# Performance work log

Measured on AMD Instinct MI355X. Metric: run time of the kernel, lower is better.

The kernel has to match this reference:

```python
import jax, jax.numpy as jnp
import numpy as np

N = 8192
D_IN = 32
HIDDEN = [32, 32, 32]   # -> 2 GraphConvolution layers
FC = [32, 1]            # hfc = [32, 32, 1] -> 2 Linear layers


def _uniform(key, shape, stdv):
    return jax.random.uniform(key, shape, jnp.float32, -stdv, stdv)


def setup_inputs() -> dict:
    key = jax.random.key(0)
    ks = jax.random.split(key, 32)
    inp = {}
    inp["V"] = jax.random.normal(ks[0], (N, D_IN), jnp.float32)
    inp["adj"] = jax.random.randint(ks[1], (N, N), 0, 4, jnp.int32)
    # GCN layer params: w1, w2, w3 [in, out], bias [out]; init U(-stdv, stdv), stdv = 1/sqrt(out)
    ki = 2
    for li in range(len(HIDDEN) - 1):
        a, b = HIDDEN[li], HIDDEN[li + 1]
        stdv = 1.0 / np.sqrt(b)
        for wname in ("w1", "w2", "w3"):
            inp[f"{wname}_{li}"] = _uniform(ks[ki], (a, b), stdv); ki += 1
        inp[f"gb_{li}"] = _uniform(ks[ki], (b,), stdv); ki += 1
    # FC params (torch Linear default init: U(-1/sqrt(in), 1/sqrt(in)))
    hfc = [HIDDEN[-1]] + FC
    for li in range(len(hfc) - 1):
        a, b = hfc[li], hfc[li + 1]
        stdv = 1.0 / np.sqrt(a)
        inp[f"fcW_{li}"] = _uniform(ks[ki], (b, a), stdv); ki += 1  # torch Linear weight is [out, in]
        inp[f"fcb_{li}"] = _uniform(ks[ki], (b,), stdv); ki += 1
    return inp


def _gcn(V, adj, w1, w2, w3, bias):
    # masked-adjacency relational aggregation: sum_k (adj==k) @ (V @ w_k)
    dt = V.dtype
    o = (adj == 1).astype(dt) @ (V @ w1)
    o = o + (adj == 2).astype(dt) @ (V @ w2)
    o = o + (adj == 3).astype(dt) @ (V @ w3)
    return jax.nn.relu(o + bias)


def reference(V, adj, w1_0, w2_0, w3_0, gb_0, w1_1, w2_1, w3_1, gb_1,
              fcW_0, fcb_0, fcW_1, fcb_1):
    Z = _gcn(V, adj, w1_0, w2_0, w3_0, gb_0)          # [N, 32]
    Z = _gcn(Z, adj, w1_1, w2_1, w3_1, gb_1)          # [N, 32]
    Z = jnp.sum(Z, axis=0)                             # [32] sum pooling over nodes
    Z = jax.nn.relu(Z @ fcW_0.T + fcb_0)               # dropout = identity (eval mode)
    Z = Z @ fcW_1.T + fcb_1                            # [1]
    return jax.nn.sigmoid(Z)
```

## Files before the change

### kernel.cpp

```cpp
#include <hip/hip_runtime.h>
#include <cmath>

#define NN 8192

typedef _Float16 half8 __attribute__((ext_vector_type(8)));
typedef float floatx4 __attribute__((ext_vector_type(4)));
typedef unsigned int uint;

template <int L2>
__global__ __launch_bounds__(256) void h_kernel(
    const float* __restrict__ X, const float* __restrict__ w1,
    const float* __restrict__ w2, const float* __restrict__ w3,
    const float* __restrict__ gbias, _Float16* __restrict__ Hfrag) {
  __shared__ float wl[32][32];
  __shared__ float Xs[64][32];
  const int tid = threadIdx.x;
  const int ch = blockIdx.y;
  const float* wsrc = (ch == 0) ? w1 : (ch == 1) ? w2 : w3;
  for (int i = tid; i < 1024; i += 256) ((float*)wl)[i] = wsrc[i];
  const size_t base = (size_t)blockIdx.x * 2048 + tid * 8;
  if (L2 == 0) {
    float4 x0 = ((const float4*)(X + base))[0];
    float4 x1 = ((const float4*)(X + base))[1];
    *((float4*)(&Xs[0][0] + tid * 8)) = x0;
    *((float4*)(&Xs[0][0] + tid * 8 + 4)) = x1;
  } else {
    float4 s0 = {0.f, 0.f, 0.f, 0.f}, s1 = {0.f, 0.f, 0.f, 0.f};
#pragma unroll
    for (int c = 0; c < 8; ++c) {
      const float4* p = (const float4*)(X + (size_t)c * NN * 32 + base);
      float4 a = p[0], b = p[1];
      s0.x += a.x; s0.y += a.y; s0.z += a.z; s0.w += a.w;
      s1.x += b.x; s1.y += b.y; s1.z += b.z; s1.w += b.w;
    }
    const int c0 = (tid * 8) & 31;
    const float4 b0 = *(const float4*)(gbias + c0);
    const float4 b1 = *(const float4*)(gbias + c0 + 4);
    s0.x += b0.x; s0.y += b0.y; s0.z += b0.z; s0.w += b0.w;
    s1.x += b1.x; s1.y += b1.y; s1.z += b1.z; s1.w += b1.w;
    s0.x = s0.x > 0.f ? s0.x : 0.f; s0.y = s0.y > 0.f ? s0.y : 0.f;
    s0.z = s0.z > 0.f ? s0.z : 0.f; s0.w = s0.w > 0.f ? s0.w : 0.f;
    s1.x = s1.x > 0.f ? s1.x : 0.f; s1.y = s1.y > 0.f ? s1.y : 0.f;
    s1.z = s1.z > 0.f ? s1.z : 0.f; s1.w = s1.w > 0.f ? s1.w : 0.f;
    *((float4*)(&Xs[0][0] + tid * 8)) = s0;
    *((float4*)(&Xs[0][0] + tid * 8 + 4)) = s1;
  }
  __syncthreads();
  const int n = tid & 31, jb = tid >> 5;
  const int j0 = blockIdx.x * 64 + jb * 8;
  const int t = j0 >> 5;
  const int lane = (n & 15) | (((j0 & 31) >> 3) << 4);
  const int tile = n >> 4;
  half8 hv;
#pragma unroll
  for (int jj = 0; jj < 8; ++jj) {
    const float4* xr = (const float4*)(&Xs[jb * 8 + jj][0]);
    float acc = 0.f;
#pragma unroll
    for (int d4 = 0; d4 < 8; ++d4) {
      float4 x = xr[d4];
      acc += x.x * wl[d4 * 4 + 0][n];
      acc += x.y * wl[d4 * 4 + 1][n];
      acc += x.z * wl[d4 * 4 + 2][n];
      acc += x.w * wl[d4 * 4 + 3][n];
    }
    hv[jj] = (_Float16)acc;
  }
  size_t idx = ((((size_t)ch * 256 + t) * 2 + tile) * 64 + lane) * 8;
  *(half8*)(Hfrag + idx) = hv;
}

__device__ __forceinline__ void phaseB_core(const uint* mk,
                                            const half8* __restrict__ Hf,
                                            float* red_raw,
                                            float* __restrict__ Zpart, int rg,
                                            int c, int tid) {
  const int w = tid >> 6, lane = tid & 63;
  const int m = lane & 15, q = lane >> 4;
  const half8* hp = Hf + (size_t)(c * 32 + w * 8) * 128 + lane;
  half8 b00 = hp[0],     b01 = hp[64];
  half8 b10 = hp[32768], b11 = hp[32768 + 64];
  half8 b20 = hp[65536], b21 = hp[65536 + 64];
  floatx4 acc00 = {0.f, 0.f, 0.f, 0.f}, acc01 = {0.f, 0.f, 0.f, 0.f};
  floatx4 acc10 = {0.f, 0.f, 0.f, 0.f}, acc11 = {0.f, 0.f, 0.f, 0.f};
#pragma unroll
  for (int tl = 0; tl < 8; ++tl) {
    half8 n00, n01, n10, n11, n20, n21;
    if (tl < 7) {
      const half8* np = hp + (tl + 1) * 128;
      n00 = np[0];     n01 = np[64];
      n10 = np[32768]; n11 = np[32768 + 64];
      n20 = np[65536]; n21 = np[65536 + 64];
    }
    const uint pk = mk[tl];
    half8 a1r0, a2r0, a3r0, a1r1, a2r1, a3r1;
#pragma unroll
    for (int i = 0; i < 8; ++i) {
      const int p0 = (pk >> (2 * i)) & 3;
      const int p1 = (pk >> (16 + 2 * i)) & 3;
      a1r0[i] = (p0 == 1) ? (_Float16)1.f : (_Float16)0.f;
      a2r0[i] = (p0 == 2) ? (_Float16)1.f : (_Float16)0.f;
      a3r0[i] = (p0 == 3) ? (_Float16)1.f : (_Float16)0.f;
      a1r1[i] = (p1 == 1) ? (_Float16)1.f : (_Float16)0.f;
      a2r1[i] = (p1 == 2) ? (_Float16)1.f : (_Float16)0.f;
      a3r1[i] = (p1 == 3) ? (_Float16)1.f : (_Float16)0.f;
    }
    acc00 = __builtin_amdgcn_mfma_f32_16x16x32_f16(a1r0, b00, acc00, 0, 0, 0);
    acc00 = __builtin_amdgcn_mfma_f32_16x16x32_f16(a2r0, b10, acc00, 0, 0, 0);
    acc00 = __builtin_amdgcn_mfma_f32_16x16x32_f16(a3r0, b20, acc00, 0, 0, 0);
    acc01 = __builtin_amdgcn_mfma_f32_16x16x32_f16(a1r0, b01, acc01, 0, 0, 0);
    acc01 = __builtin_amdgcn_mfma_f32_16x16x32_f16(a2r0, b11, acc01, 0, 0, 0);
    acc01 = __builtin_amdgcn_mfma_f32_16x16x32_f16(a3r0, b21, acc01, 0, 0, 0);
    acc10 = __builtin_amdgcn_mfma_f32_16x16x32_f16(a1r1, b00, acc10, 0, 0, 0);
    acc10 = __builtin_amdgcn_mfma_f32_16x16x32_f16(a2r1, b10, acc10, 0, 0, 0);
    acc10 = __builtin_amdgcn_mfma_f32_16x16x32_f16(a3r1, b20, acc10, 0, 0, 0);
    acc11 = __builtin_amdgcn_mfma_f32_16x16x32_f16(a1r1, b01, acc11, 0, 0, 0);
    acc11 = __builtin_amdgcn_mfma_f32_16x16x32_f16(a2r1, b11, acc11, 0, 0, 0);
    acc11 = __builtin_amdgcn_mfma_f32_16x16x32_f16(a3r1, b21, acc11, 0, 0, 0);
    if (tl < 7) {
      b00 = n00; b01 = n01; b10 = n10; b11 = n11; b20 = n20; b21 = n21;
    }
  }
  float (*red)[4][64][4] = (float (*)[4][64][4])red_raw;
#pragma unroll
  for (int r = 0; r < 4; ++r) {
    red[w][0][lane][r] = acc00[r];
    red[w][1][lane][r] = acc01[r];
    red[w][2][lane][r] = acc10[r];
    red[w][3][lane][r] = acc11[r];
  }
  __syncthreads();
  if (w == 0) {
    const int rbase = rg * 32;
#pragma unroll
    for (int r = 0; r < 4; ++r) {
      const float c00 = red[0][0][lane][r] + red[1][0][lane][r] +
                        red[2][0][lane][r] + red[3][0][lane][r];
      const float c01 = red[0][1][lane][r] + red[1][1][lane][r] +
                        red[2][1][lane][r] + red[3][1][lane][r];
      const float c10 = red[0][2][lane][r] + red[1][2][lane][r] +
                        red[2][2][lane][r] + red[3][2][lane][r];
      const float c11 = red[0][3][lane][r] + red[1][3][lane][r] +
                        red[2][3][lane][r] + red[3][3][lane][r];
      const int ro0 = rbase + q * 4 + r;
      float* zp0 = Zpart + ((size_t)c * NN + ro0) * 32;
      zp0[m] = c00;
      zp0[16 + m] = c01;
      float* zp1 = Zpart + ((size_t)c * NN + ro0 + 16) * 32;
      zp1[m] = c10;
      zp1[16 + m] = c11;
    }
  }
}

__global__ __launch_bounds__(256, 4) void agg1_kernel(
    const int* __restrict__ adj, uint* __restrict__ packed_g,
    const half8* __restrict__ Hf, float* __restrict__ Zpart) {
  __shared__ char smraw[16384];
  uint* ptile = (uint*)smraw;
  const int tid = threadIdx.x;
  const int rg = blockIdx.x >> 3, c = blockIdx.x & 7;
  const int tg = tid >> 5;
  const int qt = (tid >> 1) & 3;
  const int t4 = (tid >> 3) & 3;
  const int ih = tid & 1;
  const int byte_base = tg * 1024 + qt * 256 + t4 * 4 + ih;
  unsigned char* pb = (unsigned char*)ptile;
  const size_t gofs = (size_t)rg * 32 * NN + c * 1024 + tid * 4;
#pragma unroll
  for (int r0 = 0; r0 < 32; r0 += 8) {
    int4 a[8];
#pragma unroll
    for (int rr = 0; rr < 8; ++rr)
      a[rr] = *(const int4*)(adj + gofs + (size_t)(r0 + rr) * NN);
#pragma unroll
    for (int rr = 0; rr < 8; ++rr) {
      const int r = r0 + rr;
      const uint b = (uint)(a[rr].x & 3) | ((uint)(a[rr].y & 3) << 2) |
                     ((uint)(a[rr].z & 3) << 4) | ((uint)(a[rr].w & 3) << 6);
      pb[byte_base + (r & 15) * 16 + (r >> 4) * 2] = (unsigned char)b;
    }
  }
  __syncthreads();
  uint* pg = packed_g + (size_t)blockIdx.x * 2048;
  *(uint4*)(pg + tid * 8) = *(const uint4*)(ptile + tid * 8);
  *(uint4*)(pg + tid * 8 + 4) = *(const uint4*)(ptile + tid * 8 + 4);
  const int w = tid >> 6, lane = tid & 63;
  uint mk[8];
  *(uint4*)(mk) = *(const uint4*)(ptile + (w * 2) * 256 + lane * 4);
  *(uint4*)(mk + 4) = *(const uint4*)(ptile + (w * 2 + 1) * 256 + lane * 4);
  __syncthreads();
  phaseB_core(mk, Hf, (float*)smraw, Zpart, rg, c, tid);
}

__global__ __launch_bounds__(256, 4) void agg2_kernel(
    const uint* __restrict__ packed_g, const half8* __restrict__ Hf,
    float* __restrict__ Zpart) {
  __shared__ float red_lds[4][4][64][4];
  const int tid = threadIdx.x;
  const int rg = blockIdx.x >> 3, c = blockIdx.x & 7;
  const int w = tid >> 6, lane = tid & 63;
  const uint* pg =
      packed_g + (size_t)blockIdx.x * 2048 + (w * 2) * 256 + lane * 4;
  uint mk[8];
  *(uint4*)(mk) = *(const uint4*)(pg);
  *(uint4*)(mk + 4) = *(const uint4*)(pg + 256);
  phaseB_core(mk, Hf, (float*)red_lds, Zpart, rg, c, tid);
}

__global__ __launch_bounds__(256) void pool_kernel(
    const float* __restrict__ Zpart, const float* __restrict__ bias,
    float* __restrict__ partials) {
  const int tid = threadIdx.x;
  const int col = tid & 31, ro = tid >> 5;
  const float b = bias[col];
  float s = 0.f;
  for (int rr = 0; rr < 32; ++rr) {
    const size_t r = (size_t)blockIdx.x * 256 + ro * 32 + rr;
    float v = b;
#pragma unroll
    for (int c = 0; c < 8; ++c) v += Zpart[(size_t)c * NN * 32 + r * 32 + col];
    s += v > 0.f ? v : 0.f;
  }
  __shared__ float red[8][32];
  red[ro][col] = s;
  __syncthreads();
  if (tid < 32) {
    float t = 0.f;
#pragma unroll
    for (int i = 0; i < 8; ++i) t += red[i][tid];
    partials[(size_t)blockIdx.x * 32 + tid] = t;
  }
}

__global__ __launch_bounds__(256) void fc_kernel(
    const float* __restrict__ partials, int np, const float* __restrict__ W0,
    const float* __restrict__ b0, const float* __restrict__ W1,
    const float* __restrict__ b1, float* __restrict__ out) {
  __shared__ float acc8[8][32];
  __shared__ float z[32], y[32];
  const int tid = threadIdx.x;
  const int col = tid & 31, ch = tid >> 5;
  float s = 0.f;
  for (int i = ch; i < np; i += 8) s += partials[(size_t)i * 32 + col];
  acc8[ch][col] = s;
  __syncthreads();
  if (tid < 32) {
    float t = 0.f;
#pragma unroll
    for (int i = 0; i < 8; ++i) t += acc8[i][tid];
    z[tid] = t;
  }
  __syncthreads();
  if (tid < 32) {
    float acc = b0[tid];
    for (int n = 0; n < 32; ++n) acc += W0[tid * 32 + n] * z[n];
    y[tid] = acc > 0.f ? acc : 0.f;
  }
  __syncthreads();
  if (tid == 0) {
    float acc = b1[0];
    for (int mm = 0; mm < 32; ++mm) acc += W1[mm] * y[mm];
    out[0] = 1.f / (1.f + expf(-acc));
  }
}

extern "C" void kernel_launch(void* const* d_in, const int* in_sizes, int n_in,
                              void* d_out, int out_size, void* d_ws,
                              size_t ws_size, hipStream_t stream) {
  const float* V   = (const float*)d_in[0];
  const int*   adj = (const int*)d_in[1];
  const float *w10 = (const float*)d_in[2], *w20 = (const float*)d_in[3],
              *w30 = (const float*)d_in[4], *gb0 = (const float*)d_in[5];
  const float *w11 = (const float*)d_in[6], *w21 = (const float*)d_in[7],
              *w31 = (const float*)d_in[8], *gb1 = (const float*)d_in[9];
  const float *fW0 = (const float*)d_in[10], *fb0 = (const float*)d_in[11],
              *fW1 = (const float*)d_in[12], *fb1 = (const float*)d_in[13];
  float* out = (float*)d_out;
  char* ws = (char*)d_ws;

  _Float16* Hfrag    = (_Float16*)ws;
  float*    Zpart    = (float*)(ws + 1572864);
  float*    partials = (float*)(ws + 9961472);
  uint*     packed   = (uint*)(ws + 10223616);

  h_kernel<0><<<dim3(128, 3), 256, 0, stream>>>(V, w10, w20, w30, nullptr,
                                                Hfrag);
  agg1_kernel<<<2048, 256, 0, stream>>>(adj, packed, (const half8*)Hfrag,
                                        Zpart);
  h_kernel<1><<<dim3(128, 3), 256, 0, stream>>>(Zpart, w11, w21, w31, gb0,
                                                Hfrag);
  agg2_kernel<<<2048, 256, 0, stream>>>(packed, (const half8*)Hfrag, Zpart);
  pool_kernel<<<32, 256, 0, stream>>>(Zpart, gb1, partials);
  fc_kernel<<<1, 256, 0, stream>>>(partials, 32, fW0, fb0, fW1, fb1, out);
}
```

Measured before the change: 440.4 us.

## Split adjacency packing from aggregation and process two row groups per block

The adjacency packing, which reads the 256MB int32 adj, moves into its own pack_kernel with higher occupancy, and one shared agg_kernel now serves both layers. Each aggregation block covers 64 rows instead of 32, so every B fragment of H loaded from memory feeds twice as many MFMAs and the grid is halved. The costs are an extra launch, loss of the overlap between adj reading and MFMA work that agg1 had, and more accumulator registers and LDS per block.

```diff
diff --git a/kernel.cpp b/kernel.cpp
--- a/kernel.cpp
+++ b/kernel.cpp
@@ -70,94 +70,9 @@
   *(half8*)(Hfrag + idx) = hv;
 }
 
-__device__ __forceinline__ void phaseB_core(const uint* mk,
-                                            const half8* __restrict__ Hf,
-                                            float* red_raw,
-                                            float* __restrict__ Zpart, int rg,
-                                            int c, int tid) {
-  const int w = tid >> 6, lane = tid & 63;
-  const int m = lane & 15, q = lane >> 4;
-  const half8* hp = Hf + (size_t)(c * 32 + w * 8) * 128 + lane;
-  half8 b00 = hp[0],     b01 = hp[64];
-  half8 b10 = hp[32768], b11 = hp[32768 + 64];
-  half8 b20 = hp[65536], b21 = hp[65536 + 64];
-  floatx4 acc00 = {0.f, 0.f, 0.f, 0.f}, acc01 = {0.f, 0.f, 0.f, 0.f};
-  floatx4 acc10 = {0.f, 0.f, 0.f, 0.f}, acc11 = {0.f, 0.f, 0.f, 0.f};
-#pragma unroll
-  for (int tl = 0; tl < 8; ++tl) {
-    half8 n00, n01, n10, n11, n20, n21;
-    if (tl < 7) {
-      const half8* np = hp + (tl + 1) * 128;
-      n00 = np[0];     n01 = np[64];
-      n10 = np[32768]; n11 = np[32768 + 64];
-      n20 = np[65536]; n21 = np[65536 + 64];
-    }
-    const uint pk = mk[tl];
-    half8 a1r0, a2r0, a3r0, a1r1, a2r1, a3r1;
-#pragma unroll
-    for (int i = 0; i < 8; ++i) {
-      const int p0 = (pk >> (2 * i)) & 3;
-      const int p1 = (pk >> (16 + 2 * i)) & 3;
-      a1r0[i] = (p0 == 1) ? (_Float16)1.f : (_Float16)0.f;
-      a2r0[i] = (p0 == 2) ? (_Float16)1.f : (_Float16)0.f;
-      a3r0[i] = (p0 == 3) ? (_Float16)1.f : (_Float16)0.f;
-      a1r1[i] = (p1 == 1) ? (_Float16)1.f : (_Float16)0.f;
-      a2r1[i] = (p1 == 2) ? (_Float16)1.f : (_Float16)0.f;
-      a3r1[i] = (p1 == 3) ? (_Float16)1.f : (_Float16)0.f;
-    }
-    acc00 = __builtin_amdgcn_mfma_f32_16x16x32_f16(a1r0, b00, acc00, 0, 0, 0);
-    acc00 = __builtin_amdgcn_mfma_f32_16x16x32_f16(a2r0, b10, acc00, 0, 0, 0);
-    acc00 = __builtin_amdgcn_mfma_f32_16x16x32_f16(a3r0, b20, acc00, 0, 0, 0);
-    acc01 = __builtin_amdgcn_mfma_f32_16x16x32_f16(a1r0, b01, acc01, 0, 0, 0);
-    acc01 = __builtin_amdgcn_mfma_f32_16x16x32_f16(a2r0, b11, acc01, 0, 0, 0);
-    acc01 = __builtin_amdgcn_mfma_f32_16x16x32_f16(a3r0, b21, acc01, 0, 0, 0);
-    acc10 = __builtin_amdgcn_mfma_f32_16x16x32_f16(a1r1, b00, acc10, 0, 0, 0);
-    acc10 = __builtin_amdgcn_mfma_f32_16x16x32_f16(a2r1, b10, acc10, 0, 0, 0);
-    acc10 = __builtin_amdgcn_mfma_f32_16x16x32_f16(a3r1, b20, acc10, 0, 0, 0);
-    acc11 = __builtin_amdgcn_mfma_f32_16x16x32_f16(a1r1, b01, acc11, 0, 0, 0);
-    acc11 = __builtin_amdgcn_mfma_f32_16x16x32_f16(a2r1, b11, acc11, 0, 0, 0);
-    acc11 = __builtin_amdgcn_mfma_f32_16x16x32_f16(a3r1, b21, acc11, 0, 0, 0);
-    if (tl < 7) {
-      b00 = n00; b01 = n01; b10 = n10; b11 = n11; b20 = n20; b21 = n21;
-    }
-  }
-  float (*red)[4][64][4] = (float (*)[4][64][4])red_raw;
-#pragma unroll
-  for (int r = 0; r < 4; ++r) {
-    red[w][0][lane][r] = acc00[r];
-    red[w][1][lane][r] = acc01[r];
-    red[w][2][lane][r] = acc10[r];
-    red[w][3][lane][r] = acc11[r];
-  }
-  __syncthreads();
-  if (w == 0) {
-    const int rbase = rg * 32;
-#pragma unroll
-    for (int r = 0; r < 4; ++r) {
-      const float c00 = red[0][0][lane][r] + red[1][0][lane][r] +
-                        red[2][0][lane][r] + red[3][0][lane][r];
-      const float c01 = red[0][1][lane][r] + red[1][1][lane][r] +
-                        red[2][1][lane][r] + red[3][1][lane][r];
-      const float c10 = red[0][2][lane][r] + red[1][2][lane][r] +
-                        red[2][2][lane][r] + red[3][2][lane][r];
-      const float c11 = red[0][3][lane][r] + red[1][3][lane][r] +
-                        red[2][3][lane][r] + red[3][3][lane][r];
-      const int ro0 = rbase + q * 4 + r;
-      float* zp0 = Zpart + ((size_t)c * NN + ro0) * 32;
-      zp0[m] = c00;
-      zp0[16 + m] = c01;
-      float* zp1 = Zpart + ((size_t)c * NN + ro0 + 16) * 32;
-      zp1[m] = c10;
-      zp1[16 + m] = c11;
-    }
-  }
-}
-
-__global__ __launch_bounds__(256, 4) void agg1_kernel(
-    const int* __restrict__ adj, uint* __restrict__ packed_g,
-    const half8* __restrict__ Hf, float* __restrict__ Zpart) {
-  __shared__ char smraw[16384];
-  uint* ptile = (uint*)smraw;
+__global__ __launch_bounds__(256, 8) void pack_kernel(
+    const int* __restrict__ adj, uint* __restrict__ packed_g) {
+  __shared__ uint ptile[2048];
   const int tid = threadIdx.x;
   const int rg = blockIdx.x >> 3, c = blockIdx.x & 7;
   const int tg = tid >> 5;
@@ -185,27 +100,121 @@
   uint* pg = packed_g + (size_t)blockIdx.x * 2048;
   *(uint4*)(pg + tid * 8) = *(const uint4*)(ptile + tid * 8);
   *(uint4*)(pg + tid * 8 + 4) = *(const uint4*)(ptile + tid * 8 + 4);
-  const int w = tid >> 6, lane = tid & 63;
-  uint mk[8];
-  *(uint4*)(mk) = *(const uint4*)(ptile + (w * 2) * 256 + lane * 4);
-  *(uint4*)(mk + 4) = *(const uint4*)(ptile + (w * 2 + 1) * 256 + lane * 4);
-  __syncthreads();
-  phaseB_core(mk, Hf, (float*)smraw, Zpart, rg, c, tid);
-}
-
-__global__ __launch_bounds__(256, 4) void agg2_kernel(
+}
+
+__global__ __launch_bounds__(256, 4) void agg_kernel(
     const uint* __restrict__ packed_g, const half8* __restrict__ Hf,
     float* __restrict__ Zpart) {
-  __shared__ float red_lds[4][4][64][4];
+  __shared__ float red[4][8][64][4];
   const int tid = threadIdx.x;
   const int rg = blockIdx.x >> 3, c = blockIdx.x & 7;
   const int w = tid >> 6, lane = tid & 63;
-  const uint* pg =
-      packed_g + (size_t)blockIdx.x * 2048 + (w * 2) * 256 + lane * 4;
-  uint mk[8];
-  *(uint4*)(mk) = *(const uint4*)(pg);
-  *(uint4*)(mk + 4) = *(const uint4*)(pg + 256);
-  phaseB_core(mk, Hf, (float*)red_lds, Zpart, rg, c, tid);
+  const int m = lane & 15, q = lane >> 4;
+  const uint* pgA =
+      packed_g + ((size_t)(rg * 2) * 8 + c) * 2048 + (w * 2) * 256 + lane * 4;
+  const uint* pgB =
+      packed_g + ((size_t)(rg * 2 + 1) * 8 + c) * 2048 + (w * 2) * 256 + lane * 4;
+  uint mkA[8], mkB[8];
+  *(uint4*)(mkA) = *(const uint4*)(pgA);
+  *(uint4*)(mkA + 4) = *(const uint4*)(pgA + 256);
+  *(uint4*)(mkB) = *(const uint4*)(pgB);
+  *(uint4*)(mkB + 4) = *(const uint4*)(pgB + 256);
+  const half8* hp = Hf + (size_t)(c * 32 + w * 8) * 128 + lane;
+  half8 b00 = hp[0],     b01 = hp[64];
+  half8 b10 = hp[32768], b11 = hp[32768 + 64];
+  half8 b20 = hp[65536], b21 = hp[65536 + 64];
+  floatx4 acc[4][2];
+#pragma unroll
+  for (int g = 0; g < 4; ++g)
+#pragma unroll
+    for (int h = 0; h < 2; ++h) acc[g][h] = (floatx4){0.f, 0.f, 0.f, 0.f};
+#pragma unroll
+  for (int tl = 0; tl < 8; ++tl) {
+    half8 n00, n01, n10, n11, n20, n21;
+    if (tl < 7) {
+      const half8* np = hp + (tl + 1) * 128;
+      n00 = np[0];     n01 = np[64];
+      n10 = np[32768]; n11 = np[32768 + 64];
+      n20 = np[65536]; n21 = np[65536 + 64];
+    }
+    const uint pkA = mkA[tl], pkB = mkB[tl];
+    {
+      half8 a0, a1, a2, a3;
+#pragma unroll
+      for (int i = 0; i < 8; ++i) {
+        a0[i] = (((pkA >> (2 * i)) & 3) == 1) ? (_Float16)1.f : (_Float16)0.f;
+        a1[i] = (((pkA >> (16 + 2 * i)) & 3) == 1) ? (_Float16)1.f : (_Float16)0.f;
+        a2[i] = (((pkB >> (2 * i)) & 3) == 1) ? (_Float16)1.f : (_Float16)0.f;
+        a3[i] = (((pkB >> (16 + 2 * i)) & 3) == 1) ? (_Float16)1.f : (_Float16)0.f;
+      }
+      acc[0][0] = __builtin_amdgcn_mfma_f32_16x16x32_f16(a0, b00, acc[0][0], 0, 0, 0);
+      acc[0][1] = __builtin_amdgcn_mfma_f32_16x16x32_f16(a0, b01, acc[0][1], 0, 0, 0);
+      acc[1][0] = __builtin_amdgcn_mfma_f32_16x16x32_f16(a1, b00, acc[1][0], 0, 0, 0);
+      acc[1][1] = __builtin_amdgcn_mfma_f32_16x16x32_f16(a1, b01, acc[1][1], 0, 0, 0);
+      acc[2][0] = __builtin_amdgcn_mfma_f32_16x16x32_f16(a2, b00, acc[2][0], 0, 0, 0);
+      acc[2][1] = __builtin_amdgcn_mfma_f32_16x16x32_f16(a2, b01, acc[2][1], 0, 0, 0);
+      acc[3][0] = __builtin_amdgcn_mfma_f32_16x16x32_f16(a3, b00, acc[3][0], 0, 0, 0);
+      acc[3][1] = __builtin_amdgcn_mfma_f32_16x16x32_f16(a3, b01, acc[3][1], 0, 0, 0);
+    }
+    {
+      half8 a0, a1, a2, a3;
+#pragma unroll
+      for (int i = 0; i < 8; ++i) {
+        a0[i] = (((pkA >> (2 * i)) & 3) == 2) ? (_Float16)1.f : (_Float16)0.f;
+        a1[i] = (((pkA >> (16 + 2 * i)) & 3) == 2) ? (_Float16)1.f : (_Float16)0.f;
+        a2[i] = (((pkB >> (2 * i)) & 3) == 2) ? (_Float16)1.f : (_Float16)0.f;
+        a3[i] = (((pkB >> (16 + 2 * i)) & 3) == 2) ? (_Float16)1.f : (_Float16)0.f;
+      }
+      acc[0][0] = __builtin_amdgcn_mfma_f32_16x16x32_f16(a0, b10, acc[0][0], 0, 0, 0);
+      acc[0][1] = __builtin_amdgcn_mfma_f32_16x16x32_f16(a0, b11, acc[0][1], 0, 0, 0);
+      acc[1][0] = __builtin_amdgcn_mfma_f32_16x16x32_f16(a1, b10, acc[1][0], 0, 0, 0);
+      acc[1][1] = __builtin_amdgcn_mfma_f32_16x16x32_f16(a1, b11, acc[1][1], 0, 0, 0);
+      acc[2][0] = __builtin_amdgcn_mfma_f32_16x16x32_f16(a2, b10, acc[2][0], 0, 0, 0);
+      acc[2][1] = __builtin_amdgcn_mfma_f32_16x16x32_f16(a2, b11, acc[2][1], 0, 0, 0);
+      acc[3][0] = __builtin_amdgcn_mfma_f32_16x16x32_f16(a3, b10, acc[3][0], 0, 0, 0);
+      acc[3][1] = __builtin_amdgcn_mfma_f32_16x16x32_f16(a3, b11, acc[3][1], 0, 0, 0);
+    }
+    {
+      half8 a0, a1, a2, a3;
+#pragma unroll
+      for (int i = 0; i < 8; ++i) {
+        a0[i] = (((pkA >> (2 * i)) & 3) == 3) ? (_Float16)1.f : (_Float16)0.f;
+        a1[i] = (((pkA >> (16 + 2 * i)) & 3) == 3) ? (_Float16)1.f : (_Float16)0.f;
+        a2[i] = (((pkB >> (2 * i)) & 3) == 3) ? (_Float16)1.f : (_Float16)0.f;
+        a3[i] = (((pkB >> (16 + 2 * i)) & 3) == 3) ? (_Float16)1.f : (_Float16)0.f;
+      }
+      acc[0][0] = __builtin_amdgcn_mfma_f32_16x16x32_f16(a0, b20, acc[0][0], 0, 0, 0);
+      acc[0][1] = __builtin_amdgcn_mfma_f32_16x16x32_f16(a0, b21, acc[0][1], 0, 0, 0);
+      acc[1][0] = __builtin_amdgcn_mfma_f32_16x16x32_f16(a1, b20, acc[1][0], 0, 0, 0);
+      acc[1][1] = __builtin_amdgcn_mfma_f32_16x16x32_f16(a1, b21, acc[1][1], 0, 0, 0);
+      acc[2][0] = __builtin_amdgcn_mfma_f32_16x16x32_f16(a2, b20, acc[2][0], 0, 0, 0);
+      acc[2][1] = __builtin_amdgcn_mfma_f32_16x16x32_f16(a2, b21, acc[2][1], 0, 0, 0);
+      acc[3][0] = __builtin_amdgcn_mfma_f32_16x16x32_f16(a3, b20, acc[3][0], 0, 0, 0);
+      acc[3][1] = __builtin_amdgcn_mfma_f32_16x16x32_f16(a3, b21, acc[3][1], 0, 0, 0);
+    }
+    if (tl < 7) {
+      b00 = n00; b01 = n01; b10 = n10; b11 = n11; b20 = n20; b21 = n21;
+    }
+  }
+#pragma unroll
+  for (int g = 0; g < 4; ++g)
+#pragma unroll
+    for (int h = 0; h < 2; ++h)
+#pragma unroll
+      for (int r = 0; r < 4; ++r) red[w][g * 2 + h][lane][r] = acc[g][h][r];
+  __syncthreads();
+  {
+    const int rbase = rg * 64 + w * 16;
+#pragma unroll
+    for (int h = 0; h < 2; ++h) {
+#pragma unroll
+      for (int r = 0; r < 4; ++r) {
+        const float v = red[0][w * 2 + h][lane][r] + red[1][w * 2 + h][lane][r] +
+                        red[2][w * 2 + h][lane][r] + red[3][w * 2 + h][lane][r];
+        Zpart[((size_t)c * NN + rbase + q * 4 + r) * 32 + h * 16 + m] = v;
+      }
+    }
+  }
 }
 
 __global__ __launch_bounds__(256) void pool_kernel(
@@ -284,13 +293,13 @@
   float*    partials = (float*)(ws + 9961472);
   uint*     packed   = (uint*)(ws + 10223616);
 
+  pack_kernel<<<2048, 256, 0, stream>>>(adj, packed);
   h_kernel<0><<<dim3(128, 3), 256, 0, stream>>>(V, w10, w20, w30, nullptr,
                                                 Hfrag);
-  agg1_kernel<<<2048, 256, 0, stream>>>(adj, packed, (const half8*)Hfrag,
-                                        Zpart);
+  agg_kernel<<<1024, 256, 0, stream>>>(packed, (const half8*)Hfrag, Zpart);
   h_kernel<1><<<dim3(128, 3), 256, 0, stream>>>(Zpart, w11, w21, w31, gb0,
                                                 Hfrag);
-  agg2_kernel<<<2048, 256, 0, stream>>>(packed, (const half8*)Hfrag, Zpart);
+  agg_kernel<<<1024, 256, 0, stream>>>(packed, (const half8*)Hfrag, Zpart);
   pool_kernel<<<32, 256, 0, stream>>>(Zpart, gb1, partials);
   fc_kernel<<<1, 256, 0, stream>>>(partials, 32, fW0, fb0, fW1, fb1, out);
 }
```

Result: slower. 455.9 us (+3.5%).

## Restructure agg2 so each block reuses H fragments across four row groups

Applied to the files above, without the earlier changes.

Rewrites agg2_kernel so each block handles four row groups for one column chunk. H fragments are loaded into registers once and reused across the four groups, with all three channels' B fragments held at the same time. The grid shrinks from 2048 to 512 blocks and launch bounds drop to 2 blocks per SM to make room for the larger accumulator and B register footprint. The aim is to cut redundant global reads of H, at the cost of more register pressure, lower occupancy and a serialized LDS reduction across four passes.

```diff
diff --git a/kernel.cpp b/kernel.cpp
--- a/kernel.cpp
+++ b/kernel.cpp
@@ -50,7 +50,7 @@
   const int j0 = blockIdx.x * 64 + jb * 8;
   const int t = j0 >> 5;
   const int lane = (n & 15) | (((j0 & 31) >> 3) << 4);
-  const int tile = n >> 4;
+  const int h = n >> 4;
   half8 hv;
 #pragma unroll
   for (int jj = 0; jj < 8; ++jj) {
@@ -66,7 +66,7 @@
     }
     hv[jj] = (_Float16)acc;
   }
-  size_t idx = ((((size_t)ch * 256 + t) * 2 + tile) * 64 + lane) * 8;
+  size_t idx = ((((size_t)ch * 256 + t) * 2 + h) * 64 + lane) * 8;
   *(half8*)(Hfrag + idx) = hv;
 }
 
@@ -193,19 +193,92 @@
   phaseB_core(mk, Hf, (float*)smraw, Zpart, rg, c, tid);
 }
 
-__global__ __launch_bounds__(256, 4) void agg2_kernel(
+__global__ __launch_bounds__(256, 2) void agg2_kernel(
     const uint* __restrict__ packed_g, const half8* __restrict__ Hf,
     float* __restrict__ Zpart) {
-  __shared__ float red_lds[4][4][64][4];
-  const int tid = threadIdx.x;
-  const int rg = blockIdx.x >> 3, c = blockIdx.x & 7;
+  __shared__ float red[4][2][2][64][4];
+  const int tid = threadIdx.x;
   const int w = tid >> 6, lane = tid & 63;
-  const uint* pg =
-      packed_g + (size_t)blockIdx.x * 2048 + (w * 2) * 256 + lane * 4;
-  uint mk[8];
-  *(uint4*)(mk) = *(const uint4*)(pg);
-  *(uint4*)(mk + 4) = *(const uint4*)(pg + 256);
-  phaseB_core(mk, Hf, (float*)red_lds, Zpart, rg, c, tid);
+  const int m = lane & 15, q = lane >> 4;
+  const int c = blockIdx.x >> 6, rgb = blockIdx.x & 63;
+  floatx4 acc[4][2][2];
+#pragma unroll
+  for (int u = 0; u < 4; ++u)
+#pragma unroll
+    for (int g = 0; g < 2; ++g)
+#pragma unroll
+      for (int h = 0; h < 2; ++h) acc[u][g][h] = (floatx4){0.f, 0.f, 0.f, 0.f};
+#pragma unroll
+  for (int tp = 0; tp < 2; ++tp) {
+    const int tg = w + tp * 4;
+    const half8* hp = Hf + (size_t)(c * 32 + tg * 4) * 128 + lane;
+    half8 B[3][4][2];
+#pragma unroll
+    for (int ch = 0; ch < 3; ++ch)
+#pragma unroll
+      for (int t4 = 0; t4 < 4; ++t4) {
+        B[ch][t4][0] = hp[ch * 32768 + t4 * 128];
+        B[ch][t4][1] = hp[ch * 32768 + t4 * 128 + 64];
+      }
+    uint4 mk[4];
+#pragma unroll
+    for (int u = 0; u < 4; ++u)
+      mk[u] = *(const uint4*)(packed_g +
+                              ((size_t)(rgb * 4 + u) * 8 + c) * 2048 +
+                              tg * 256 + lane * 4);
+#pragma unroll
+    for (int u = 0; u < 4; ++u) {
+      const uint mka[4] = {mk[u].x, mk[u].y, mk[u].z, mk[u].w};
+#pragma unroll
+      for (int t4 = 0; t4 < 4; ++t4) {
+        const uint pk = mka[t4];
+#pragma unroll
+        for (int ch = 0; ch < 3; ++ch) {
+          half8 a0, a1;
+#pragma unroll
+          for (int i = 0; i < 8; ++i) {
+            a0[i] = (((pk >> (2 * i)) & 3) == ch + 1) ? (_Float16)1.f
+                                                      : (_Float16)0.f;
+            a1[i] = (((pk >> (16 + 2 * i)) & 3) == ch + 1) ? (_Float16)1.f
+                                                           : (_Float16)0.f;
+          }
+          acc[u][0][0] = __builtin_amdgcn_mfma_f32_16x16x32_f16(
+              a0, B[ch][t4][0], acc[u][0][0], 0, 0, 0);
+          acc[u][0][1] = __builtin_amdgcn_mfma_f32_16x16x32_f16(
+              a0, B[ch][t4][1], acc[u][0][1], 0, 0, 0);
+          acc[u][1][0] = __builtin_amdgcn_mfma_f32_16x16x32_f16(
+              a1, B[ch][t4][0], acc[u][1][0], 0, 0, 0);
+          acc[u][1][1] = __builtin_amdgcn_mfma_f32_16x16x32_f16(
+              a1, B[ch][t4][1], acc[u][1][1], 0, 0, 0);
+        }
+      }
+    }
+  }
+#pragma unroll
+  for (int u = 0; u < 4; ++u) {
+    __syncthreads();
+#pragma unroll
+    for (int g = 0; g < 2; ++g)
+#pragma unroll
+      for (int h = 0; h < 2; ++h)
+#pragma unroll
+        for (int r = 0; r < 4; ++r) red[w][g][h][lane][r] = acc[u][g][h][r];
+    __syncthreads();
+    if (w == 0) {
+      const int rbase = rgb * 128 + u * 32;
+#pragma unroll
+      for (int g = 0; g < 2; ++g)
+#pragma unroll
+        for (int h = 0; h < 2; ++h)
+#pragma unroll
+          for (int r = 0; r < 4; ++r) {
+            const float v = red[0][g][h][lane][r] + red[1][g][h][lane][r] +
+                            red[2][g][h][lane][r] + red[3][g][h][lane][r];
+            const int row = rbase + g * 16 + q * 4 + r;
+            Zpart[((size_t)c * NN + row) * 32 + h * 16 + m] = v;
+          }
+    }
+  }
 }
 
 __global__ __launch_bounds__(256) void pool_kernel(
@@ -290,7 +363,7 @@
                                         Zpart);
   h_kernel<1><<<dim3(128, 3), 256, 0, stream>>>(Zpart, w11, w21, w31, gb0,
                                                 Hfrag);
-  agg2_kernel<<<2048, 256, 0, stream>>>(packed, (const half8*)Hfrag, Zpart);
+  agg2_kernel<<<512, 256, 0, stream>>>(packed, (const half8*)Hfrag, Zpart);
   pool_kernel<<<32, 256, 0, stream>>>(Zpart, gb1, partials);
   fc_kernel<<<1, 256, 0, stream>>>(partials, 32, fW0, fb0, fW1, fb1, out);
 }
```

After: 442.7 us. Within noise of the previous version (+0.5%).
